# Kernel tuning notes

Measured on AMD Instinct MI355X. Metric: run time of the kernel, lower is better.

## Reference

```python
import jax, jax.numpy as jnp
import numpy as np

LN_EPS = 1e-5


def setup_inputs() -> dict:
    key = jax.random.key(0)
    ks = jax.random.split(key, 6)
    B, N, C, H = 8, 4096, 768, 12
    D = C // H
    x = jax.random.normal(ks[0], (B, N, C), dtype=jnp.float32)
    w_qkv = jax.random.normal(ks[1], (3 * C, C), dtype=jnp.float32) * (C ** -0.5)
    w_proj = jax.random.normal(ks[2], (C, C), dtype=jnp.float32) * (C ** -0.5)
    b_proj = jnp.zeros((C,), dtype=jnp.float32)
    # trunc_normal_(std=0.02) approximated by clipped normal
    p1 = jnp.clip(jax.random.normal(ks[3], (H, N), dtype=jnp.float32) * 0.02, -0.04, 0.04)
    p2 = jnp.clip(jax.random.normal(ks[4], (H, N), dtype=jnp.float32) * 0.02, -0.04, 0.04)
    gamma = jnp.ones((D,), dtype=jnp.float32)
    beta = jnp.zeros((D,), dtype=jnp.float32)
    return {"x": x, "w_qkv": w_qkv, "w_proj": w_proj, "b_proj": b_proj,
            "p1": p1, "p2": p2, "gamma": gamma, "beta": beta}


def _layernorm(h, gamma, beta):
    mu = jnp.mean(h, axis=-1, keepdims=True)
    var = jnp.var(h, axis=-1, keepdims=True)
    return (h - mu) * jax.lax.rsqrt(var + LN_EPS) * gamma + beta


def reference(x, w_qkv, w_proj, b_proj, p1, p2, gamma, beta):
    B, N, C = x.shape
    H = p1.shape[0]
    D = C // H
    # qkv projection (no bias): [B,N,3C] -> [3,B,H,N,D]
    qkv = (x @ w_qkv.T).reshape(B, N, 3, H, D).transpose(2, 0, 3, 1, 4)
    q, k, v = qkv[0], qkv[1], qkv[2]
    # weighted k*v reduction over sequence: [B,H,D]
    modulator = jnp.einsum('hn,bhnd->bhd', p2, k * v)
    modulator = _layernorm(modulator, gamma, beta)
    # broadcast modulation back over N: [B,H,N,D]
    modulator = jnp.einsum('hn,bhd->bhnd', p1, modulator)
    out = (q * modulator).transpose(0, 2, 1, 3).reshape(B, N, C)
    return out @ w_proj.T + b_proj
```

## Files before the change

### kernel.cpp

```cpp
#include <hip/hip_runtime.h>
#include <stdint.h>
#include <stddef.h>

#define LN_EPS 1e-5f

typedef __bf16 bf16;
typedef __bf16 bf16x8 __attribute__((ext_vector_type(8)));
typedef __bf16 bf16x4 __attribute__((ext_vector_type(4)));
typedef float f32x4 __attribute__((ext_vector_type(4)));

#define GL16(gp, lp)                                                                   \
  __builtin_amdgcn_global_load_lds((__attribute__((address_space(1))) uint32_t*)(gp),  \
                                   (__attribute__((address_space(3))) uint32_t*)(lp),  \
                                   16, 0, 0)

#define SBAR   asm volatile("s_barrier" ::: "memory")
#define VMW(N) asm volatile("s_waitcnt vmcnt(" #N ")" ::: "memory")
#define LGK(N) asm volatile("s_waitcnt lgkmcnt(" #N ")" ::: "memory")
#define SCB    __builtin_amdgcn_sched_barrier(0)
#define SP1    __builtin_amdgcn_s_setprio(1)
#define SP0    __builtin_amdgcn_s_setprio(0)
#define NOWAIT ((void)0)

#define XV4   6291456
#define WQV4  442368
#define WPV4  147456
__global__ __launch_bounds__(256) void cvt_all(const float* __restrict__ x,
                                               const float* __restrict__ wq,
                                               const float* __restrict__ wp,
                                               bf16* __restrict__ xb,
                                               bf16* __restrict__ wqb,
                                               bf16* __restrict__ wpb) {
  int i = blockIdx.x * 256 + threadIdx.x;
  const float* src; bf16* dst; int off;
  if (i < XV4)              { src = x;  dst = xb;  off = i; }
  else if (i < XV4 + WQV4)  { src = wq; dst = wqb; off = i - XV4; }
  else                      { src = wp; dst = wpb; off = i - (XV4 + WQV4); }
  const float4 v = ((const float4*)src)[off];
  bf16x4 o;
  o[0] = (bf16)v.x; o[1] = (bf16)v.y; o[2] = (bf16)v.z; o[3] = (bf16)v.w;
  ((bf16x4*)dst)[off] = o;
}

#define STAGE_A(T, H) do {                                              \
    bf16* d_ = ldsA + ((((T)&1) << 1) + (H)) * 8192 + tid8;             \
    GL16(pA + (H) * 98304 + (T) * 64, d_);                              \
    GL16(pA + (H) * 98304 + 49152 + (T) * 64, d_ + 4096); } while (0)

#define STAGE_B(T, H) do {                                              \
    bf16* d_ = ldsB + ((((T)&1) << 1) + (H)) * 8192 + tid8;             \
    GL16(pB##H##0 + (T) * 64, d_);                                      \
    GL16(pB##H##1 + (T) * 64, d_ + 4096); } while (0)

#define RD_AQ(D, MQ) do {                                               \
    _Pragma("unroll") for (int mf = 0; mf < 4; ++mf) {                  \
      const int r_ = (MQ) * 64 + mf * 16 + l16;                         \
      const bf16* b_ = ldsA + (((D) << 1) + wm) * 8192 + r_ * 64;       \
      const int x_ = r_ & 7;                                            \
      aF[mf][0] = *(const bf16x8*)(b_ + ((qg ^ x_) << 3));              \
      aF[mf][1] = *(const bf16x8*)(b_ + (((4 + qg) ^ x_) << 3));        \
    } } while (0)

#define RD_BQ(D, NQ, BF) do {                                           \
    _Pragma("unroll") for (int nf = 0; nf < 2; ++nf) {                  \
      const int r_ = hn64 + (NQ) * 32 + nf * 16 + l16;                  \
      const bf16* b_ = ldsB + (((D) << 1) + hb) * 8192 + r_ * 64;       \
      const int x_ = r_ & 7;                                            \
      BF[nf][0] = *(const bf16x8*)(b_ + ((qg ^ x_) << 3));              \
      BF[nf][1] = *(const bf16x8*)(b_ + (((4 + qg) ^ x_) << 3));        \
    } } while (0)

#define MMQ(MQ, NQ, BF) do {                                            \
    _Pragma("unroll") for (int mf = 0; mf < 4; ++mf)                    \
      _Pragma("unroll") for (int nf = 0; nf < 2; ++nf) {                \
        acc[(MQ)*4+mf][(NQ)*2+nf] = __builtin_amdgcn_mfma_f32_16x16x32_bf16( \
            aF[mf][0], BF[nf][0], acc[(MQ)*4+mf][(NQ)*2+nf], 0, 0, 0);  \
        acc[(MQ)*4+mf][(NQ)*2+nf] = __builtin_amdgcn_mfma_f32_16x16x32_bf16( \
            aF[mf][1], BF[nf][1], acc[(MQ)*4+mf][(NQ)*2+nf], 0, 0, 0);  \
      } } while (0)

#define ITER(T, P12, P38, WV4, WV8) do {                                       \
     RD_AQ(0, 0); RD_BQ(0, 0, bF0); if (P12) STAGE_A((T)+1, 0); LGK(8);\
    SBAR; LGK(0); SCB; SP1; MMQ(0, 0, bF0); SP0; SBAR;                         \
     RD_BQ(0, 1, bF1); if (P12) STAGE_A((T)+1, 1);                     \
    SBAR; LGK(0); SCB; SP1; MMQ(0, 1, bF1); SP0; SBAR;                         \
     RD_AQ(0, 1); if (P38) STAGE_B((T)+2, 0);                          \
    SBAR; LGK(0); SCB; SP1; MMQ(1, 0, bF0); SP0; SBAR;                         \
     if (P38) STAGE_B((T)+2, 1);                                       \
    SBAR; LGK(0); SCB; SP1; MMQ(1, 1, bF1); SP0; WV4; SBAR;                    \
     RD_AQ(1, 0); RD_BQ(1, 0, bF0); if (P38) STAGE_A((T)+2, 0); LGK(8);\
    SBAR; LGK(0); SCB; SP1; MMQ(0, 0, bF0); SP0; SBAR;                         \
     RD_BQ(1, 1, bF1); if (P38) STAGE_A((T)+2, 1);                     \
    SBAR; LGK(0); SCB; SP1; MMQ(0, 1, bF1); SP0; SBAR;                         \
     RD_AQ(1, 1); if (P38) STAGE_B((T)+3, 0);                          \
    SBAR; LGK(0); SCB; SP1; MMQ(1, 0, bF0); SP0; SBAR;                         \
     if (P38) STAGE_B((T)+3, 1);                                       \
    SBAR; LGK(0); SCB; SP1; MMQ(1, 1, bF1); SP0; WV8; SBAR;                    \
  } while (0)

__device__ __forceinline__ void gemm256(const bf16* pA,
                                        const bf16* pB00, const bf16* pB01,
                                        const bf16* pB10, const bf16* pB11,
                                        bf16* sh, f32x4 acc[8][4]) {
  const int tid  = threadIdx.x;
  const int lane = tid & 63;
  const int wave = tid >> 6;
  const int wm   = wave >> 2;
  const int wn   = wave & 3;
  const int hb   = wn >> 1;
  const int hn64 = (wn & 1) * 64;
  const int l16  = lane & 15;
  const int qg   = lane >> 4;
  const int tid8 = tid * 8;
  bf16* const ldsA = sh;
  bf16* const ldsB = sh + 32768;
  bf16x8 aF[4][2], bF0[2][2], bF1[2][2];

  STAGE_A(0, 0); STAGE_A(0, 1); STAGE_B(0, 0); STAGE_B(0, 1);
  STAGE_A(1, 0); STAGE_A(1, 1); STAGE_B(1, 0); STAGE_B(1, 1);
  VMW(8);
  SBAR;

  ITER(0, 0, 1, VMW(4), VMW(4));
#pragma unroll 1
  for (int T = 2; T <= 8; T += 2) {
    ITER(T, 1, 1, VMW(4), VMW(4));
  }
  ITER(10, 1, 0, VMW(0), NOWAIT);

  __syncthreads();
}

__global__ __launch_bounds__(512, 2) void kv_gemm_reduce(const bf16* __restrict__ A,
                                                         const bf16* __restrict__ B,
                                                         const float* __restrict__ p2,
                                                         float* __restrict__ partials) {
  __shared__ __align__(16) bf16 sh[66560];
  __shared__ float red[4][2][64];

  const int lin  = blockIdx.y * 6 + blockIdx.x;
  const int xcd  = lin & 7;
  const int j    = lin >> 3;
  const int hh   = j % 6;
  const int mblk = xcd + 8 * (j / 6);
  const int m0   = mblk * 256;
  const int h0   = hh * 2;

  const int tid = threadIdx.x;
  const int tr  = tid >> 3;
  const int tc  = ((tid & 7) ^ ((tid >> 3) & 7)) * 8;
  const bf16* pA   = A + (size_t)(m0 + tr) * 768 + tc;
  const bf16* pB00 = B + (size_t)(768  + (h0 + 0) * 64 + tr) * 768 + tc;
  const bf16* pB01 = B + (size_t)(1536 + (h0 + 0) * 64 + tr) * 768 + tc;
  const bf16* pB10 = B + (size_t)(768  + (h0 + 1) * 64 + tr) * 768 + tc;
  const bf16* pB11 = B + (size_t)(1536 + (h0 + 1) * 64 + tr) * 768 + tc;

  f32x4 acc[8][4] = {};
  gemm256(pA, pB00, pB01, pB10, pB11, sh, acc);

  const int lane = tid & 63, wave = tid >> 6;
  const int wm = wave >> 2, wn = wave & 3, l16 = lane & 15, qg = lane >> 4;
  const int r0s = wm * 128 + qg * 4;
  const int c0s = wn * 64 + l16;
#pragma unroll
  for (int mi = 0; mi < 8; ++mi)
#pragma unroll
    for (int ni = 0; ni < 4; ++ni)
#pragma unroll
      for (int r = 0; r < 4; ++r)
        sh[(size_t)(r0s + mi * 16 + r) * 260 + c0s + ni * 16] = (bf16)acc[mi][ni][r];
  __syncthreads();

  const int nq = tid >> 7, hl = (tid >> 6) & 1, d = tid & 63;
  const float4* pw4 = (const float4*)(p2 + (size_t)(h0 + hl) * 4096 + (m0 & 4095) + nq * 64);
  const bf16* pk = sh + (size_t)(nq * 64) * 260 + hl * 128 + d;
  const bf16* pv = pk + 64;
  float s = 0.f;
#pragma unroll
  for (int nb = 0; nb < 16; ++nb) {
    const float4 w = pw4[nb];
    const int n = nb * 4;
    s += w.x * (float)pk[(n + 0) * 260] * (float)pv[(n + 0) * 260]
       + w.y * (float)pk[(n + 1) * 260] * (float)pv[(n + 1) * 260]
       + w.z * (float)pk[(n + 2) * 260] * (float)pv[(n + 2) * 260]
       + w.w * (float)pk[(n + 3) * 260] * (float)pv[(n + 3) * 260];
  }
  red[nq][hl][d] = s;
  __syncthreads();
  if (tid < 128) {
    const int hx = tid >> 6, dd = tid & 63;
    partials[((size_t)mblk * 12 + h0 + hx) * 64 + dd] =
        red[0][hx][dd] + red[1][hx][dd] + red[2][hx][dd] + red[3][hx][dd];
  }
}

__global__ __launch_bounds__(64) void mod_reduce_ln(const float* __restrict__ partials,
                                                    const float* __restrict__ gamma,
                                                    const float* __restrict__ beta,
                                                    float* __restrict__ mod) {
  const int h = blockIdx.x, b = blockIdx.y;
  const int d = threadIdx.x;

  const float* p = partials + ((size_t)(b * 16) * 12 + h) * 64 + d;
  float s = 0.f;
#pragma unroll
  for (int mb = 0; mb < 16; ++mb) s += p[(size_t)mb * 12 * 64];

  float sum = s, sumsq = s * s;
#pragma unroll
  for (int o = 32; o > 0; o >>= 1) {
    sum   += __shfl_xor(sum, o);
    sumsq += __shfl_xor(sumsq, o);
  }
  const float mu  = sum * (1.f / 64.f);
  const float var = sumsq * (1.f / 64.f) - mu * mu;
  const float r   = rsqrtf(var + LN_EPS);
  mod[(b * 12 + h) * 64 + d] = (s - mu) * r * gamma[d] + beta[d];
}

__global__ __launch_bounds__(512, 2) void q_gemm_mod(const bf16* __restrict__ A,
                                                     const bf16* __restrict__ B,
                                                     const float* __restrict__ p1,
                                                     const float* __restrict__ mod,
                                                     bf16* __restrict__ amod) {
  __shared__ __align__(16) bf16 sh[65536];

  const int lin  = blockIdx.y * 3 + blockIdx.x;
  const int xcd  = lin & 7;
  const int j    = lin >> 3;
  const int nblk = j % 3;
  const int mblk = xcd + 8 * (j / 3);
  const int n0   = nblk * 256;
  const int m0   = mblk * 256;

  const int tid = threadIdx.x;
  const int tr  = tid >> 3;
  const int tc  = ((tid & 7) ^ ((tid >> 3) & 7)) * 8;
  const bf16* pA   = A + (size_t)(m0 + tr) * 768 + tc;
  const bf16* pB00 = B + (size_t)(n0 + tr) * 768 + tc;
  const bf16* pB01 = pB00 + (size_t)64 * 768;
  const bf16* pB10 = pB00 + (size_t)128 * 768;
  const bf16* pB11 = pB00 + (size_t)192 * 768;

  f32x4 acc[8][4] = {};
  gemm256(pA, pB00, pB01, pB10, pB11, sh, acc);

  const int lane = tid & 63, wave = tid >> 6;
  const int wm = wave >> 2, wn = wave & 3, l16 = lane & 15;
  const int row0 = m0 + wm * 128 + (lane >> 4) * 4;
  const int col0 = n0 + wn * 64 + l16;
  const int b    = m0 >> 12;
  const int h    = (n0 >> 6) + wn;

  float p1v[8][4];
#pragma unroll
  for (int mi = 0; mi < 8; ++mi)
#pragma unroll
    for (int r = 0; r < 4; ++r)
      p1v[mi][r] = p1[(size_t)h * 4096 + ((row0 + mi * 16 + r) & 4095)];
  float mv[4];
#pragma unroll
  for (int ni = 0; ni < 4; ++ni) mv[ni] = mod[b * 768 + col0 + ni * 16];

#pragma unroll
  for (int mi = 0; mi < 8; ++mi)
#pragma unroll
    for (int ni = 0; ni < 4; ++ni)
#pragma unroll
      for (int r = 0; r < 4; ++r)
        amod[(size_t)(row0 + mi * 16 + r) * 768 + col0 + ni * 16] =
            (bf16)(acc[mi][ni][r] * p1v[mi][r] * mv[ni]);
}

__global__ __launch_bounds__(512, 2) void gemm_proj(const bf16* __restrict__ A,
                                                    const bf16* __restrict__ B,
                                                    const float* __restrict__ bias,
                                                    float* __restrict__ C) {
  __shared__ __align__(16) bf16 sh[65536];

  const int lin  = blockIdx.y * 3 + blockIdx.x;
  const int xcd  = lin & 7;
  const int j    = lin >> 3;
  const int nblk = j % 3;
  const int mblk = xcd + 8 * (j / 3);
  const int n0   = nblk * 256;
  const int m0   = mblk * 256;

  const int tid = threadIdx.x;
  const int tr  = tid >> 3;
  const int tc  = ((tid & 7) ^ ((tid >> 3) & 7)) * 8;
  const bf16* pA   = A + (size_t)(m0 + tr) * 768 + tc;
  const bf16* pB00 = B + (size_t)(n0 + tr) * 768 + tc;
  const bf16* pB01 = pB00 + (size_t)64 * 768;
  const bf16* pB10 = pB00 + (size_t)128 * 768;
  const bf16* pB11 = pB00 + (size_t)192 * 768;

  f32x4 acc[8][4] = {};
  gemm256(pA, pB00, pB01, pB10, pB11, sh, acc);

  const int lane = tid & 63, wave = tid >> 6;
  const int wm = wave >> 2, wn = wave & 3, l16 = lane & 15;
  const int row0 = m0 + wm * 128 + (lane >> 4) * 4;
  const int col0 = n0 + wn * 64 + l16;
#pragma unroll
  for (int ni = 0; ni < 4; ++ni) {
    const int col = col0 + ni * 16;
    const float bv = bias[col];
#pragma unroll
    for (int mi = 0; mi < 8; ++mi)
#pragma unroll
      for (int r = 0; r < 4; ++r)
        C[(size_t)(row0 + mi * 16 + r) * 768 + col] = acc[mi][ni][r] + bv;
  }
}

extern "C" void kernel_launch(void* const* d_in, const int* in_sizes, int n_in,
                              void* d_out, int out_size, void* d_ws, size_t ws_size,
                              hipStream_t stream) {
  (void)in_sizes; (void)n_in; (void)out_size; (void)ws_size;

  const float* x      = (const float*)d_in[0];
  const float* w_qkv  = (const float*)d_in[1];
  const float* w_proj = (const float*)d_in[2];
  const float* b_proj = (const float*)d_in[3];
  const float* p1     = (const float*)d_in[4];
  const float* p2     = (const float*)d_in[5];
  const float* gamma  = (const float*)d_in[6];
  const float* beta   = (const float*)d_in[7];
  float* out = (float*)d_out;

  char* ws = (char*)d_ws;
  bf16*  xb       = (bf16*)(ws + 0);
  bf16*  wqb      = (bf16*)(ws + 50331648);
  bf16*  wpb      = (bf16*)(ws + 53870592);
  bf16*  amod     = (bf16*)(ws + 55050240);
  float* partials = (float*)(ws + 105381888);
  float* mod      = (float*)(ws + 106168320);

  cvt_all<<<26880, 256, 0, stream>>>(x, w_qkv, w_proj, xb, wqb, wpb);

  kv_gemm_reduce<<<dim3(6, 128), 512, 0, stream>>>(xb, wqb, p2, partials);

  mod_reduce_ln<<<dim3(12, 8), 64, 0, stream>>>(partials, gamma, beta, mod);

  q_gemm_mod<<<dim3(3, 128), 512, 0, stream>>>(xb, wqb, p1, mod, amod);

  gemm_proj<<<dim3(3, 128), 512, 0, stream>>>(amod, wpb, b_proj, out);
}
```

Baseline: 372.8 us.

## Reduce k*v in registers and use 128x256 tiles for q and proj GEMMs

The kv GEMM now permutes the weight rows it loads so that each wave's accumulators hold matching k and v columns. The p2-weighted k*v product can then be formed and reduced directly in registers with lane shuffles, which removes the bf16 round trip through shared memory and one barrier. The q-modulation and projection GEMMs move to a new 128x256 tile pipeline, doubling the grid to 768 blocks and shrinking LDS, which should improve load balance across CUs at the cost of reloading B tiles more often. A full waitcnt is also added at the end of the GEMM helpers.

```diff
diff --git a/kernel.cpp b/kernel.cpp
--- a/kernel.cpp
+++ b/kernel.cpp
@@ -128,6 +128,97 @@
   }
   ITER(10, 1, 0, VMW(0), NOWAIT);
 
+  asm volatile("s_waitcnt vmcnt(0) lgkmcnt(0)" ::: "memory");
+  __syncthreads();
+}
+
+#define QSTAGE_A(T) do {                                          \
+    bf16* d_ = qldsA + (((T)&1)) * 8192 + tid8;                   \
+    GL16(qA + (T) * 64, d_);                                      \
+    GL16(qA + 49152 + (T) * 64, d_ + 4096); } while (0)
+
+#define QSTAGE_B(T, H) do {                                       \
+    bf16* d_ = qldsB + ((((T)&1) << 1) + (H)) * 8192 + tid8;      \
+    GL16(qB##H##0 + (T) * 64, d_);                                \
+    GL16(qB##H##1 + (T) * 64, d_ + 4096); } while (0)
+
+#define QRD_A(D, MQ) do {                                         \
+    _Pragma("unroll") for (int mf = 0; mf < 2; ++mf) {            \
+      const int r_ = wm * 64 + (MQ) * 32 + mf * 16 + l16;         \
+      const bf16* b_ = qldsA + (D) * 8192 + r_ * 64;              \
+      const int x_ = r_ & 7;                                      \
+      aF[mf][0] = *(const bf16x8*)(b_ + ((qg ^ x_) << 3));        \
+      aF[mf][1] = *(const bf16x8*)(b_ + (((4 + qg) ^ x_) << 3));  \
+    } } while (0)
+
+#define QRD_B(D, NQ, BF) do {                                     \
+    _Pragma("unroll") for (int nf = 0; nf < 2; ++nf) {            \
+      const int r_ = hn64 + (NQ) * 32 + nf * 16 + l16;            \
+      const bf16* b_ = qldsB + (((D) << 1) + hb) * 8192 + r_ * 64;\
+      const int x_ = r_ & 7;                                      \
+      BF[nf][0] = *(const bf16x8*)(b_ + ((qg ^ x_) << 3));        \
+      BF[nf][1] = *(const bf16x8*)(b_ + (((4 + qg) ^ x_) << 3));  \
+    } } while (0)
+
+#define QMM(MQ, NQ, BF) do {                                      \
+    _Pragma("unroll") for (int mf = 0; mf < 2; ++mf)              \
+      _Pragma("unroll") for (int nf = 0; nf < 2; ++nf) {          \
+        acc[(MQ)*2+mf][(NQ)*2+nf] = __builtin_amdgcn_mfma_f32_16x16x32_bf16( \
+            aF[mf][0], BF[nf][0], acc[(MQ)*2+mf][(NQ)*2+nf], 0, 0, 0); \
+        acc[(MQ)*2+mf][(NQ)*2+nf] = __builtin_amdgcn_mfma_f32_16x16x32_bf16( \
+            aF[mf][1], BF[nf][1], acc[(MQ)*2+mf][(NQ)*2+nf], 0, 0, 0); \
+      } } while (0)
+
+#define QITER(T, P1, P38, WVp4, WVp8) do {                                     \
+     QRD_A(0, 0); QRD_B(0, 0, bF0); if (P1) QSTAGE_A((T)+1);           \
+    SBAR; LGK(0); SCB; SP1; QMM(0, 0, bF0); SP0; SBAR;                         \
+     QRD_B(0, 1, bF1);                                                 \
+    SBAR; LGK(0); SCB; SP1; QMM(0, 1, bF1); SP0; SBAR;                         \
+     QRD_A(0, 1); if (P38) QSTAGE_B((T)+2, 0);                         \
+    SBAR; LGK(0); SCB; SP1; QMM(1, 0, bF0); SP0; SBAR;                         \
+     if (P38) QSTAGE_B((T)+2, 1);                                      \
+    SBAR; LGK(0); SCB; SP1; QMM(1, 1, bF1); SP0; WVp4; SBAR;                   \
+     QRD_A(1, 0); QRD_B(1, 0, bF0); if (P38) QSTAGE_A((T)+2);          \
+    SBAR; LGK(0); SCB; SP1; QMM(0, 0, bF0); SP0; SBAR;                         \
+     QRD_B(1, 1, bF1);                                                 \
+    SBAR; LGK(0); SCB; SP1; QMM(0, 1, bF1); SP0; SBAR;                         \
+     QRD_A(1, 1); if (P38) QSTAGE_B((T)+3, 0);                         \
+    SBAR; LGK(0); SCB; SP1; QMM(1, 0, bF0); SP0; SBAR;                         \
+     if (P38) QSTAGE_B((T)+3, 1);                                      \
+    SBAR; LGK(0); SCB; SP1; QMM(1, 1, bF1); SP0; WVp8; SBAR;                   \
+  } while (0)
+
+__device__ __forceinline__ void gemm128x256(const bf16* qA,
+                                            const bf16* qB00, const bf16* qB01,
+                                            const bf16* qB10, const bf16* qB11,
+                                            bf16* sh, f32x4 acc[4][4]) {
+  const int tid  = threadIdx.x;
+  const int lane = tid & 63;
+  const int wave = tid >> 6;
+  const int wm   = wave >> 2;
+  const int wn   = wave & 3;
+  const int hb   = wn >> 1;
+  const int hn64 = (wn & 1) * 64;
+  const int l16  = lane & 15;
+  const int qg   = lane >> 4;
+  const int tid8 = tid * 8;
+  bf16* const qldsA = sh;
+  bf16* const qldsB = sh + 16384;
+  bf16x8 aF[2][2], bF0[2][2], bF1[2][2];
+
+  QSTAGE_A(0); QSTAGE_B(0, 0); QSTAGE_B(0, 1);
+  QSTAGE_A(1); QSTAGE_B(1, 0); QSTAGE_B(1, 1);
+  VMW(6);
+  SBAR;
+
+  QITER(0, 0, 1, VMW(4), VMW(4));
+#pragma unroll 1
+  for (int T = 2; T <= 8; T += 2) {
+    QITER(T, 1, 1, VMW(4), VMW(4));
+  }
+  QITER(10, 1, 0, VMW(0), NOWAIT);
+
+  asm volatile("s_waitcnt vmcnt(0) lgkmcnt(0)" ::: "memory");
   __syncthreads();
 }
 
@@ -135,8 +226,8 @@
                                                          const bf16* __restrict__ B,
                                                          const float* __restrict__ p2,
                                                          float* __restrict__ partials) {
-  __shared__ __align__(16) bf16 sh[66560];
-  __shared__ float red[4][2][64];
+  __shared__ __align__(16) bf16 sh[65536];
+  __shared__ float red2[2][4][2][16];
 
   const int lin  = blockIdx.y * 6 + blockIdx.x;
   const int xcd  = lin & 7;
@@ -149,48 +240,40 @@
   const int tid = threadIdx.x;
   const int tr  = tid >> 3;
   const int tc  = ((tid & 7) ^ ((tid >> 3) & 7)) * 8;
-  const bf16* pA   = A + (size_t)(m0 + tr) * 768 + tc;
-  const bf16* pB00 = B + (size_t)(768  + (h0 + 0) * 64 + tr) * 768 + tc;
-  const bf16* pB01 = B + (size_t)(1536 + (h0 + 0) * 64 + tr) * 768 + tc;
-  const bf16* pB10 = B + (size_t)(768  + (h0 + 1) * 64 + tr) * 768 + tc;
-  const bf16* pB11 = B + (size_t)(1536 + (h0 + 1) * 64 + tr) * 768 + tc;
+  const bf16* pA = A + (size_t)(m0 + tr) * 768 + tc;
+#define WQROW(r) (768 + (((r) >> 4) & 1) * 768 + (h0 + ((r) >> 7)) * 64 + \
+                  ((((r) >> 5) & 3) * 16 + ((r) & 15)))
+  const bf16* pB00 = B + (size_t)WQROW(tr) * 768 + tc;
+  const bf16* pB01 = B + (size_t)WQROW(64 + tr) * 768 + tc;
+  const bf16* pB10 = B + (size_t)WQROW(128 + tr) * 768 + tc;
+  const bf16* pB11 = B + (size_t)WQROW(192 + tr) * 768 + tc;
+#undef WQROW
 
   f32x4 acc[8][4] = {};
   gemm256(pA, pB00, pB01, pB10, pB11, sh, acc);
 
   const int lane = tid & 63, wave = tid >> 6;
   const int wm = wave >> 2, wn = wave & 3, l16 = lane & 15, qg = lane >> 4;
-  const int r0s = wm * 128 + qg * 4;
-  const int c0s = wn * 64 + l16;
-#pragma unroll
-  for (int mi = 0; mi < 8; ++mi)
-#pragma unroll
-    for (int ni = 0; ni < 4; ++ni)
-#pragma unroll
-      for (int r = 0; r < 4; ++r)
-        sh[(size_t)(r0s + mi * 16 + r) * 260 + c0s + ni * 16] = (bf16)acc[mi][ni][r];
-  __syncthreads();
-
-  const int nq = tid >> 7, hl = (tid >> 6) & 1, d = tid & 63;
-  const float4* pw4 = (const float4*)(p2 + (size_t)(h0 + hl) * 4096 + (m0 & 4095) + nq * 64);
-  const bf16* pk = sh + (size_t)(nq * 64) * 260 + hl * 128 + d;
-  const bf16* pv = pk + 64;
-  float s = 0.f;
-#pragma unroll
-  for (int nb = 0; nb < 16; ++nb) {
-    const float4 w = pw4[nb];
-    const int n = nb * 4;
-    s += w.x * (float)pk[(n + 0) * 260] * (float)pv[(n + 0) * 260]
-       + w.y * (float)pk[(n + 1) * 260] * (float)pv[(n + 1) * 260]
-       + w.z * (float)pk[(n + 2) * 260] * (float)pv[(n + 2) * 260]
-       + w.w * (float)pk[(n + 3) * 260] * (float)pv[(n + 3) * 260];
-  }
-  red[nq][hl][d] = s;
+  const float* p2h = p2 + (size_t)(h0 + (wn >> 1)) * 4096 + (m0 & 4095) + wm * 128;
+  float s0 = 0.f, s1 = 0.f;
+#pragma unroll
+  for (int ai = 0; ai < 8; ++ai) {
+    const float4 w = *(const float4*)(p2h + ai * 16 + qg * 4);
+    s0 += w.x * acc[ai][0][0] * acc[ai][1][0] + w.y * acc[ai][0][1] * acc[ai][1][1]
+        + w.z * acc[ai][0][2] * acc[ai][1][2] + w.w * acc[ai][0][3] * acc[ai][1][3];
+    s1 += w.x * acc[ai][2][0] * acc[ai][3][0] + w.y * acc[ai][2][1] * acc[ai][3][1]
+        + w.z * acc[ai][2][2] * acc[ai][3][2] + w.w * acc[ai][2][3] * acc[ai][3][3];
+  }
+  s0 += __shfl_xor(s0, 16); s0 += __shfl_xor(s0, 32);
+  s1 += __shfl_xor(s1, 16); s1 += __shfl_xor(s1, 32);
+  if (qg == 0) { red2[wm][wn][0][l16] = s0; red2[wm][wn][1][l16] = s1; }
   __syncthreads();
   if (tid < 128) {
-    const int hx = tid >> 6, dd = tid & 63;
-    partials[((size_t)mblk * 12 + h0 + hx) * 64 + dd] =
-        red[0][hx][dd] + red[1][hx][dd] + red[2][hx][dd] + red[3][hx][dd];
+    const int l = tid & 15, jj = (tid >> 4) & 1, wnn = tid >> 5;
+    const float v = red2[0][wnn][jj][l] + red2[1][wnn][jj][l];
+    const int hx = h0 + (wnn >> 1);
+    const int dd = ((wnn & 1) * 2 + jj) * 16 + l;
+    partials[((size_t)mblk * 12 + hx) * 64 + dd] = v;
   }
 }
 
@@ -223,7 +306,7 @@
                                                      const float* __restrict__ p1,
                                                      const float* __restrict__ mod,
                                                      bf16* __restrict__ amod) {
-  __shared__ __align__(16) bf16 sh[65536];
+  __shared__ __align__(16) bf16 sh[49152];
 
   const int lin  = blockIdx.y * 3 + blockIdx.x;
   const int xcd  = lin & 7;
@@ -231,52 +314,52 @@
   const int nblk = j % 3;
   const int mblk = xcd + 8 * (j / 3);
   const int n0   = nblk * 256;
-  const int m0   = mblk * 256;
+  const int m0   = mblk * 128;
 
   const int tid = threadIdx.x;
   const int tr  = tid >> 3;
   const int tc  = ((tid & 7) ^ ((tid >> 3) & 7)) * 8;
-  const bf16* pA   = A + (size_t)(m0 + tr) * 768 + tc;
-  const bf16* pB00 = B + (size_t)(n0 + tr) * 768 + tc;
-  const bf16* pB01 = pB00 + (size_t)64 * 768;
-  const bf16* pB10 = pB00 + (size_t)128 * 768;
-  const bf16* pB11 = pB00 + (size_t)192 * 768;
-
-  f32x4 acc[8][4] = {};
-  gemm256(pA, pB00, pB01, pB10, pB11, sh, acc);
+  const bf16* qA   = A + (size_t)(m0 + tr) * 768 + tc;
+  const bf16* qB00 = B + (size_t)(n0 + tr) * 768 + tc;
+  const bf16* qB01 = qB00 + (size_t)64 * 768;
+  const bf16* qB10 = qB00 + (size_t)128 * 768;
+  const bf16* qB11 = qB00 + (size_t)192 * 768;
+
+  f32x4 acc[4][4] = {};
+  gemm128x256(qA, qB00, qB01, qB10, qB11, sh, acc);
 
   const int lane = tid & 63, wave = tid >> 6;
-  const int wm = wave >> 2, wn = wave & 3, l16 = lane & 15;
-  const int row0 = m0 + wm * 128 + (lane >> 4) * 4;
+  const int wm = wave >> 2, wn = wave & 3, l16 = lane & 15, qg = lane >> 4;
+  const int row0 = m0 + wm * 64 + qg * 4;
   const int col0 = n0 + wn * 64 + l16;
   const int b    = m0 >> 12;
   const int h    = (n0 >> 6) + wn;
 
-  float p1v[8][4];
-#pragma unroll
-  for (int mi = 0; mi < 8; ++mi)
+  float p1v[4][4];
+#pragma unroll
+  for (int ai = 0; ai < 4; ++ai)
 #pragma unroll
     for (int r = 0; r < 4; ++r)
-      p1v[mi][r] = p1[(size_t)h * 4096 + ((row0 + mi * 16 + r) & 4095)];
+      p1v[ai][r] = p1[(size_t)h * 4096 + ((row0 + ai * 16 + r) & 4095)];
   float mv[4];
 #pragma unroll
-  for (int ni = 0; ni < 4; ++ni) mv[ni] = mod[b * 768 + col0 + ni * 16];
-
-#pragma unroll
-  for (int mi = 0; mi < 8; ++mi)
-#pragma unroll
-    for (int ni = 0; ni < 4; ++ni)
+  for (int bj = 0; bj < 4; ++bj) mv[bj] = mod[b * 768 + col0 + bj * 16];
+
+#pragma unroll
+  for (int ai = 0; ai < 4; ++ai)
+#pragma unroll
+    for (int bj = 0; bj < 4; ++bj)
 #pragma unroll
       for (int r = 0; r < 4; ++r)
-        amod[(size_t)(row0 + mi * 16 + r) * 768 + col0 + ni * 16] =
-            (bf16)(acc[mi][ni][r] * p1v[mi][r] * mv[ni]);
+        amod[(size_t)(row0 + ai * 16 + r) * 768 + col0 + bj * 16] =
+            (bf16)(acc[ai][bj][r] * p1v[ai][r] * mv[bj]);
 }
 
 __global__ __launch_bounds__(512, 2) void gemm_proj(const bf16* __restrict__ A,
                                                     const bf16* __restrict__ B,
                                                     const float* __restrict__ bias,
                                                     float* __restrict__ C) {
-  __shared__ __align__(16) bf16 sh[65536];
+  __shared__ __align__(16) bf16 sh[49152];
 
   const int lin  = blockIdx.y * 3 + blockIdx.x;
   const int xcd  = lin & 7;
@@ -284,33 +367,33 @@
   const int nblk = j % 3;
   const int mblk = xcd + 8 * (j / 3);
   const int n0   = nblk * 256;
-  const int m0   = mblk * 256;
+  const int m0   = mblk * 128;
 
   const int tid = threadIdx.x;
   const int tr  = tid >> 3;
   const int tc  = ((tid & 7) ^ ((tid >> 3) & 7)) * 8;
-  const bf16* pA   = A + (size_t)(m0 + tr) * 768 + tc;
-  const bf16* pB00 = B + (size_t)(n0 + tr) * 768 + tc;
-  const bf16* pB01 = pB00 + (size_t)64 * 768;
-  const bf16* pB10 = pB00 + (size_t)128 * 768;
-  const bf16* pB11 = pB00 + (size_t)192 * 768;
-
-  f32x4 acc[8][4] = {};
-  gemm256(pA, pB00, pB01, pB10, pB11, sh, acc);
+  const bf16* qA   = A + (size_t)(m0 + tr) * 768 + tc;
+  const bf16* qB00 = B + (size_t)(n0 + tr) * 768 + tc;
+  const bf16* qB01 = qB00 + (size_t)64 * 768;
+  const bf16* qB10 = qB00 + (size_t)128 * 768;
+  const bf16* qB11 = qB00 + (size_t)192 * 768;
+
+  f32x4 acc[4][4] = {};
+  gemm128x256(qA, qB00, qB01, qB10, qB11, sh, acc);
 
   const int lane = tid & 63, wave = tid >> 6;
-  const int wm = wave >> 2, wn = wave & 3, l16 = lane & 15;
-  const int row0 = m0 + wm * 128 + (lane >> 4) * 4;
+  const int wm = wave >> 2, wn = wave & 3, l16 = lane & 15, qg = lane >> 4;
+  const int row0 = m0 + wm * 64 + qg * 4;
   const int col0 = n0 + wn * 64 + l16;
 #pragma unroll
-  for (int ni = 0; ni < 4; ++ni) {
-    const int col = col0 + ni * 16;
+  for (int bj = 0; bj < 4; ++bj) {
+    const int col = col0 + bj * 16;
     const float bv = bias[col];
 #pragma unroll
-    for (int mi = 0; mi < 8; ++mi)
+    for (int ai = 0; ai < 4; ++ai)
 #pragma unroll
       for (int r = 0; r < 4; ++r)
-        C[(size_t)(row0 + mi * 16 + r) * 768 + col] = acc[mi][ni][r] + bv;
+        C[(size_t)(row0 + ai * 16 + r) * 768 + col] = acc[ai][bj][r] + bv;
   }
 }
 
@@ -343,7 +426,7 @@
 
   mod_reduce_ln<<<dim3(12, 8), 64, 0, stream>>>(partials, gamma, beta, mod);
 
-  q_gemm_mod<<<dim3(3, 128), 512, 0, stream>>>(xb, wqb, p1, mod, amod);
-
-  gemm_proj<<<dim3(3, 128), 512, 0, stream>>>(amod, wpb, b_proj, out);
-}
+  q_gemm_mod<<<dim3(3, 256), 512, 0, stream>>>(xb, wqb, p1, mod, amod);
+
+  gemm_proj<<<dim3(3, 256), 512, 0, stream>>>(amod, wpb, b_proj, out);
+}
```

Measured after the change: 355.6 us. -4.6%, faster.
